# Kernel tuning notes

Hardware: AMD Instinct MI355X
Metric: run time of the kernel (lower is better)

## Reference

```python
import jax, jax.numpy as jnp
import numpy as np

B, S, HID = 2, 2048, 2048
NH = 16
HD = HID // NH  # 128


def setup_inputs() -> dict:
    key = jax.random.key(0)
    ks = jax.random.split(key, 12)
    sc = 0.02
    return {
        "hidden_state": jax.random.normal(ks[0], (B, S, HID), jnp.float32),
        "attention_mask": jax.random.uniform(ks[1], (B, 1, S, S), jnp.float32),
        "Wq": jax.random.normal(ks[2], (HID, HID), jnp.float32) * sc,
        "bq": jnp.zeros((HID,), jnp.float32),
        "Wk": jax.random.normal(ks[3], (HD, HID), jnp.float32) * sc,
        "bk": jnp.zeros((HD,), jnp.float32),
        "Wv": jax.random.normal(ks[4], (HD, HID), jnp.float32) * sc,
        "bv": jnp.zeros((HD,), jnp.float32),
        "Wo": jax.random.normal(ks[5], (HID, HID), jnp.float32) * sc,
        "bo": jnp.zeros((HID,), jnp.float32),
    }


def reference(hidden_state, attention_mask, Wq, bq, Wk, bk, Wv, bv, Wo, bo):
    b = hidden_state.shape[0]
    # projections (nn.Linear: x @ W.T + b)
    q = hidden_state @ Wq.T + bq                      # [B,S,HID]
    k = hidden_state @ Wk.T + bk                      # [B,S,HD] (single shared head)
    v = hidden_state @ Wv.T + bv                      # [B,S,HD]
    # split heads: q -> [B,NH,S,HD]
    q = q.reshape(b, -1, NH, HD).transpose(0, 2, 1, 3)
    scale = jnp.sqrt(jnp.asarray(HD, q.dtype))
    scores = jnp.einsum('bhsd,btd->bhst', q, k) / scale  # [B,NH,S,S]
    # faithful to source: mask scaled by -1e-09 (as written)
    scores = scores + attention_mask * (-1e-09)
    probs = jax.nn.softmax(scores, axis=-1)
    out = jnp.einsum('bhst,btd->bhsd', probs, v)          # [B,NH,S,HD]
    # faithful to source: transpose(-1,-2) then flat view to [B,S,HID]
    out = out.transpose(0, 1, 3, 2).reshape(b, -1, HD * NH)
    return out @ Wo.T + bo
```

## Files before the change

kernel.cpp:

```cpp
#include <hip/hip_runtime.h>
#include <hip/hip_bf16.h>

#define BATCH 2
#define SEQ 2048
#define HIDDIM 2048
#define NHEADS 16
#define HDIM 128
#define QKVN 2304

typedef __attribute__((ext_vector_type(8))) short bf16x8;
typedef __attribute__((ext_vector_type(4))) short short4v;
typedef __attribute__((ext_vector_type(4))) float f32x4;
typedef __attribute__((ext_vector_type(16))) float f32x16;
typedef __attribute__((ext_vector_type(4))) unsigned u32x4;

__device__ __forceinline__ short f2bf(float f) {
  unsigned u = __builtin_bit_cast(unsigned, f);
  unsigned r = (u + 0x7fffu + ((u >> 16) & 1u)) >> 16;
  return (short)r;
}

__device__ __forceinline__ unsigned cvtpk_bf16(float a, float b) {
  unsigned r;
  asm("v_cvt_pk_bf16_f32 %0, %1, %2" : "=v"(r) : "v"(a), "v"(b));
  return r;
}

#define PLSWAP(a, b) asm("v_permlane32_swap_b32 %0, %1" : "+v"(a), "+v"(b))

__device__ __forceinline__ void gl_lds16(const void* g, void* l) {
  __builtin_amdgcn_global_load_lds(
      (const __attribute__((address_space(1))) void*)g,
      (__attribute__((address_space(3))) void*)l, 16, 0, 0);
}

__device__ __forceinline__ float max3f(float a, float b, float c) {
  return fmaxf(fmaxf(a, b), c);
}
__device__ __forceinline__ float vmax16(const f32x16& v) {
  float a = max3f(v[0], v[1], v[2]);
  float b = max3f(v[3], v[4], v[5]);
  float c = max3f(v[6], v[7], v[8]);
  float d = max3f(v[9], v[10], v[11]);
  float e = max3f(v[12], v[13], v[14]);
  return fmaxf(max3f(a, b, c), max3f(d, e, v[15]));
}

__global__ void prep_kernel(const float* __restrict__ h, const float* __restrict__ Wq,
                            const float* __restrict__ Wk, const float* __restrict__ Wv,
                            const float* __restrict__ Wo,
                            const float* __restrict__ bq, const float* __restrict__ bk,
                            const float* __restrict__ bv,
                            short* __restrict__ h_bf, short* __restrict__ Wqkv_bf,
                            short* __restrict__ Wo_bf, float* __restrict__ bqkv)
{
  int bid = blockIdx.x;
  const float* src;
  short* dst;
  int n;
  if (bid < 8192)        { src = h;  dst = h_bf;                n = 8388608; }
  else if (bid < 12288)  { src = Wq; dst = Wqkv_bf;             n = 4194304; bid -= 8192; }
  else if (bid < 12544)  { src = Wk; dst = Wqkv_bf + 4194304;   n = 262144;  bid -= 12288; }
  else if (bid < 12800)  { src = Wv; dst = Wqkv_bf + 4456448;   n = 262144;  bid -= 12544; }
  else if (bid < 12809) {
    int i = (bid - 12800) * 256 + threadIdx.x;
    if (i < QKVN) {
      float v;
      if (i < HIDDIM) v = bq[i];
      else if (i < HIDDIM + HDIM) v = bk[i - HIDDIM];
      else v = bv[i - HIDDIM - HDIM];
      bqkv[i] = v;
    }
    return;
  }
  else                   { src = Wo; dst = Wo_bf;               n = 4194304; bid -= 12809; }
  int i = (bid * 256 + threadIdx.x) * 4;
  if (i >= n) return;
  float4 v = *(const float4*)(src + i);
  short4v o;
  o[0] = f2bf(v.x); o[1] = f2bf(v.y); o[2] = f2bf(v.z); o[3] = f2bf(v.w);
  *(short4v*)(dst + i) = o;
}

__global__ void cvt_kernel(const float* __restrict__ in, short* __restrict__ out, int n) {
  int i = (blockIdx.x * blockDim.x + threadIdx.x) * 4;
  if (i >= n) return;
  float4 v = *(const float4*)(in + i);
  short4v o;
  o[0] = f2bf(v.x); o[1] = f2bf(v.y); o[2] = f2bf(v.z); o[3] = f2bf(v.w);
  *(short4v*)(out + i) = o;
}

template <int MODE>
__global__ __launch_bounds__(256, 2)
void gemm_bt(const short* __restrict__ A, const short* __restrict__ W,
             const float* __restrict__ bias, void* __restrict__ Cv, void* __restrict__ Cv2,
             int M, int N, int K, long sA, long sC)
{
  __shared__ short As[128 * 64];
  __shared__ short Ws[128 * 64];
  const int tid = threadIdx.x;
  const int lane = tid & 63;
  const int w = tid >> 6;
  const int wr = w >> 1, wc = w & 1;
  const int tm = blockIdx.y * 128, tn = blockIdx.x * 128;
  const short* Ap = A + (size_t)blockIdx.z * sA;

  const int rA = lane & 15;
  const int r7 = rA & 7;
  const int srow = lane >> 3;
  const int scg  = (lane & 7) ^ srow;

  f32x4 acc[4][4] = {};

  for (int k0 = 0; k0 < K; k0 += 64) {
    __syncthreads();
#pragma unroll
    for (int i = 0; i < 4; ++i) {
      int ch = w * 4 + i;
      gl_lds16(Ap + (size_t)(tm + ch * 8 + srow) * K + k0 + scg * 8, As + ch * 512);
      gl_lds16(W  + (size_t)(tn + ch * 8 + srow) * K + k0 + scg * 8, Ws + ch * 512);
    }
    __syncthreads();
#pragma unroll
    for (int kk = 0; kk < 64; kk += 32) {
      const int cg = (kk >> 3) + (lane >> 4);
      const int co = ((cg ^ r7) << 3);
      bf16x8 af[4];
#pragma unroll
      for (int mi = 0; mi < 4; ++mi)
        af[mi] = *(const bf16x8*)(As + ((wr * 64 + mi * 16 + rA) << 6) + co);
#pragma unroll
      for (int ni = 0; ni < 4; ++ni) {
        bf16x8 wf = *(const bf16x8*)(Ws + ((wc * 64 + ni * 16 + rA) << 6) + co);
#pragma unroll
        for (int mi = 0; mi < 4; ++mi)
          acc[mi][ni] = __builtin_amdgcn_mfma_f32_16x16x32_bf16(af[mi], wf, acc[mi][ni], 0, 0, 0);
      }
    }
  }

  const float QSCALE = 0.12752600954427384f;
  const int cr = (lane >> 4) * 4;
  const int cc = lane & 15;
#pragma unroll
  for (int ni = 0; ni < 4; ++ni) {
    int col = tn + wc * 64 + ni * 16 + cc;
    float bv = bias[col];
#pragma unroll
    for (int mi = 0; mi < 4; ++mi) {
#pragma unroll
      for (int r = 0; r < 4; ++r) {
        int row = tm + wr * 64 + mi * 16 + cr + r;
        float v = acc[mi][ni][r] + bv;
        if constexpr (MODE == 0) {
          ((float*)Cv)[(size_t)blockIdx.z * sC + (size_t)row * N + col] = v;
        } else {
          if (col < HIDDIM)
            ((short*)Cv)[(size_t)row * QKVN + col] = f2bf(v * QSCALE);
          else if (col < HIDDIM + HDIM)
            ((short*)Cv)[(size_t)row * QKVN + col] = f2bf(v);
          else
            ((short*)Cv2)[(size_t)(col - HIDDIM - HDIM) * (BATCH * SEQ) + row] = f2bf(v);
        }
      }
    }
  }
}

__global__ __launch_bounds__(256, 2)
void attn_kernel(const short* __restrict__ QKV, const short* __restrict__ Vt,
                 short* __restrict__ OT)
{
  __shared__ short smem[32768];
  short* Ks = smem;
  short* Vs = smem + 16384;
  const int tid = threadIdx.x;
  const int l31 = tid & 31;
  const int hi2 = (tid >> 5) & 1;
  const int w = tid >> 6;
  const int b = blockIdx.z, h = blockIdx.y, qt = blockIdx.x;
  const int rx = l31 & 15;
  const short* Kp = QKV + HIDDIM;

  const short* kptr[8];
  const short* vptr[8];
  {
    const int rin = (tid & 63) >> 4;
    const int gp = tid & 15;
#pragma unroll
    for (int i = 0; i < 8; ++i) {
      int ch = w * 8 + i;
      int row = ch * 4 + rin;
      int gl = gp ^ (row & 15);
      kptr[i] = Kp + (size_t)(b * SEQ + row) * QKVN + gl * 8;
      vptr[i] = Vt + (size_t)row * (BATCH * SEQ) + b * SEQ + gl * 8;
    }
  }

  bf16x8 qf[8];
  {
    const short* Qp = QKV + (size_t)(b * SEQ + qt * 128 + w * 32 + l31) * QKVN + h * HDIM;
#pragma unroll
    for (int kk = 0; kk < 8; ++kk)
      qf[kk] = *(const bf16x8*)(Qp + kk * 16 + hi2 * 8);
  }

  f32x16 o[4] = {};
  float m = -1e30f, l = 0.f;

  for (int c = 0; c < 16; ++c) {
    __syncthreads();
#pragma unroll
    for (int i = 0; i < 8; ++i) {
      int ch = w * 8 + i;
      gl_lds16(kptr[i], Ks + ch * 512);
      gl_lds16(vptr[i], Vs + ch * 512);
      kptr[i] += 128 * QKVN;
      vptr[i] += 128;
    }
    __syncthreads();

    f32x16 s[4] = {};
    __builtin_amdgcn_s_setprio(1);
#pragma unroll
    for (int n = 0; n < 4; ++n) {
      const int row = n * 32 + l31;
#pragma unroll
      for (int kk = 0; kk < 8; ++kk) {
        bf16x8 kf = *(const bf16x8*)(Ks + row * 128 + (((kk * 2 + hi2) ^ rx) << 3));
        s[n] = __builtin_amdgcn_mfma_f32_32x32x16_bf16(kf, qf[kk], s[n], 0, 0, 0);
      }
    }
    __builtin_amdgcn_s_setprio(0);

    float mx = fmaxf(fmaxf(vmax16(s[0]), vmax16(s[1])),
                     fmaxf(vmax16(s[2]), vmax16(s[3])));
    mx = fmaxf(mx, __shfl_xor(mx, 32));
    if (!__all(mx <= m + 8.f)) {
      float mn = fmaxf(m, mx);
      float cf = __builtin_amdgcn_exp2f(m - mn);
      m = mn; l *= cf;
#pragma unroll
      for (int nd = 0; nd < 4; ++nd)
#pragma unroll
        for (int r = 0; r < 16; ++r) o[nd][r] *= cf;
    }

    float rs = 0.f;
#pragma unroll
    for (int n = 0; n < 4; ++n) {
      float p[16];
#pragma unroll
      for (int r = 0; r < 16; ++r)
        p[r] = __builtin_amdgcn_exp2f(s[n][r] - m);
      rs += (((p[0] + p[1]) + (p[2] + p[3])) + ((p[4] + p[5]) + (p[6] + p[7])))
          + (((p[8] + p[9]) + (p[10] + p[11])) + ((p[12] + p[13]) + (p[14] + p[15])));
      unsigned w0 = cvtpk_bf16(p[0], p[1]),  w1 = cvtpk_bf16(p[2], p[3]);
      unsigned w2 = cvtpk_bf16(p[4], p[5]),  w3 = cvtpk_bf16(p[6], p[7]);
      unsigned w4 = cvtpk_bf16(p[8], p[9]),  w5 = cvtpk_bf16(p[10], p[11]);
      unsigned w6 = cvtpk_bf16(p[12], p[13]), w7 = cvtpk_bf16(p[14], p[15]);
      PLSWAP(w0, w2); PLSWAP(w1, w3);
      PLSWAP(w4, w6); PLSWAP(w5, w7);
      bf16x8 pa0 = __builtin_bit_cast(bf16x8, (u32x4){w0, w1, w2, w3});
      bf16x8 pa1 = __builtin_bit_cast(bf16x8, (u32x4){w4, w5, w6, w7});
      __builtin_amdgcn_s_setprio(1);
#pragma unroll
      for (int nd = 0; nd < 4; ++nd) {
        const int row = nd * 32 + l31;
        bf16x8 vf0 = *(const bf16x8*)(Vs + row * 128 + ((((n * 2) * 2 + hi2) ^ rx) << 3));
        o[nd] = __builtin_amdgcn_mfma_f32_32x32x16_bf16(vf0, pa0, o[nd], 0, 0, 0);
        bf16x8 vf1 = *(const bf16x8*)(Vs + row * 128 + ((((n * 2 + 1) * 2 + hi2) ^ rx) << 3));
        o[nd] = __builtin_amdgcn_mfma_f32_32x32x16_bf16(vf1, pa1, o[nd], 0, 0, 0);
      }
      __builtin_amdgcn_s_setprio(0);
    }
    rs += __shfl_xor(rs, 32);
    l += rs;
  }

  const float inv = 1.f / l;
  short* dst = OT + (size_t)b * (SEQ * HIDDIM) + (size_t)(h * HDIM) * SEQ
             + qt * 128 + w * 32 + l31;
#pragma unroll
  for (int nd = 0; nd < 4; ++nd) {
#pragma unroll
    for (int r = 0; r < 16; ++r) {
      int d = nd * 32 + (r & 3) + 8 * (r >> 2) + 4 * hi2;
      dst[(size_t)d * SEQ] = f2bf(o[nd][r] * inv);
    }
  }
}

extern "C" void kernel_launch(void* const* d_in, const int* in_sizes, int n_in,
                              void* d_out, int out_size, void* d_ws, size_t ws_size,
                              hipStream_t stream)
{
  const float* hidden = (const float*)d_in[0];
  const float* Wq = (const float*)d_in[2];
  const float* bq = (const float*)d_in[3];
  const float* Wk = (const float*)d_in[4];
  const float* bk = (const float*)d_in[5];
  const float* Wv = (const float*)d_in[6];
  const float* bv = (const float*)d_in[7];
  const float* Wo = (const float*)d_in[8];
  const float* bo = (const float*)d_in[9];
  float* out = (float*)d_out;

  short* ws      = (short*)d_ws;
  short* QKV     = ws;
  short* Vt_bf   = ws + 9437184;
  short* h_bf    = Vt_bf + 524288;
  short* OT      = h_bf;
  short* Wqkv_bf = h_bf + 8388608;
  float* bqkv    = (float*)(Wqkv_bf + 4718592);
  short* Wo_sep  = (short*)(bqkv + QKVN);

  const bool sep = ws_size >= (size_t)54535168;
  short* Wo_bf = sep ? Wo_sep : QKV;

  prep_kernel<<<sep ? 16905 : 12809, 256, 0, stream>>>(
      hidden, Wq, Wk, Wv, Wo, bq, bk, bv, h_bf, Wqkv_bf, Wo_bf, bqkv);

  gemm_bt<3><<<dim3(18, 32, 1), 256, 0, stream>>>(h_bf, Wqkv_bf, bqkv, QKV, Vt_bf,
                                                  4096, QKVN, 2048, 0, 0);
  attn_kernel<<<dim3(16, 16, 2), 256, 0, stream>>>(QKV, Vt_bf, OT);
  if (!sep) cvt_kernel<<<4096, 256, 0, stream>>>(Wo, Wo_bf, 4194304);
  gemm_bt<0><<<dim3(16, 16, 2), 256, 0, stream>>>(OT, Wo_bf, bo, out, nullptr,
                                                  2048, 2048, 2048, 4194304, 4194304);
}
```

Baseline: 188.3 us.

## Pipeline attention with triple-buffered 64-key tiles and 256-row query blocks

The attention kernel now uses 512-thread blocks that each cover 256 query rows, so every loaded K/V tile feeds twice as many rows. The key loop steps in 64-key tiles through a three-slot LDS ring, and it is software-pipelined: the next tile's load and the next QK^T run while softmax and PV run on the current tile. This aims to hide global-to-LDS latency and halve K/V reloads per query. The cost is more LDS (96KB per block), more registers for the second score set, and half as many blocks in the grid.

```diff
diff --git a/kernel.cpp b/kernel.cpp
--- a/kernel.cpp
+++ b/kernel.cpp
@@ -168,14 +168,13 @@
   }
 }
 
-__global__ __launch_bounds__(256, 2)
+__global__ __launch_bounds__(512, 2)
 void attn_kernel(const short* __restrict__ QKV, const short* __restrict__ Vt,
                  short* __restrict__ OT)
 {
-  __shared__ short smem[32768];
-  short* Ks = smem;
-  short* Vs = smem + 16384;
+  __shared__ short smem[49152];
   const int tid = threadIdx.x;
+  const int lane = tid & 63;
   const int l31 = tid & 31;
   const int hi2 = (tid >> 5) & 1;
   const int w = tid >> 6;
@@ -183,105 +182,132 @@
   const int rx = l31 & 15;
   const short* Kp = QKV + HIDDIM;
 
-  const short* kptr[8];
-  const short* vptr[8];
+  const short *kp0, *kp1, *vp0, *vp1;
+  int dK0, dK1, dV0, dV1;
   {
-    const int rin = (tid & 63) >> 4;
-    const int gp = tid & 15;
-#pragma unroll
-    for (int i = 0; i < 8; ++i) {
-      int ch = w * 8 + i;
-      int row = ch * 4 + rin;
-      int gl = gp ^ (row & 15);
-      kptr[i] = Kp + (size_t)(b * SEQ + row) * QKVN + gl * 8;
-      vptr[i] = Vt + (size_t)row * (BATCH * SEQ) + b * SEQ + gl * 8;
-    }
+    int s0 = w * 128 + lane, s1 = s0 + 64;
+    int r0 = s0 >> 4, g0 = (s0 & 15) ^ (r0 & 15);
+    int r1 = s1 >> 4, g1 = (s1 & 15) ^ (r1 & 15);
+    kp0 = Kp + (size_t)(b * SEQ + r0) * QKVN + g0 * 8;
+    kp1 = Kp + (size_t)(b * SEQ + r1) * QKVN + g1 * 8;
+    int d0 = (g0 >> 3) * 64 + r0, e0 = g0 & 7;
+    int d1 = (g1 >> 3) * 64 + r1, e1 = g1 & 7;
+    vp0 = Vt + (size_t)d0 * (BATCH * SEQ) + b * SEQ + e0 * 8;
+    vp1 = Vt + (size_t)d1 * (BATCH * SEQ) + b * SEQ + e1 * 8;
+    dK0 = w * 1024;        dK1 = dK0 + 512;
+    dV0 = 8192 + dK0;      dV1 = 8192 + dK1;
   }
 
   bf16x8 qf[8];
   {
-    const short* Qp = QKV + (size_t)(b * SEQ + qt * 128 + w * 32 + l31) * QKVN + h * HDIM;
+    const short* Qp = QKV + (size_t)(b * SEQ + qt * 256 + w * 32 + l31) * QKVN + h * HDIM;
 #pragma unroll
     for (int kk = 0; kk < 8; ++kk)
       qf[kk] = *(const bf16x8*)(Qp + kk * 16 + hi2 * 8);
   }
 
   f32x16 o[4] = {};
+  f32x16 sA[2], sB[2];
   float m = -1e30f, l = 0.f;
 
-  for (int c = 0; c < 16; ++c) {
+#define STAGE(BUF)                                                         \
+  { short* nb = smem + (BUF) * 16384;                                      \
+    gl_lds16(kp0, nb + dK0); gl_lds16(kp1, nb + dK1);                      \
+    gl_lds16(vp0, nb + dV0); gl_lds16(vp1, nb + dV1);                      \
+    kp0 += 64 * QKVN; kp1 += 64 * QKVN; vp0 += 64; vp1 += 64; }
+
+#define QKT(SN, BUF)                                                       \
+  { const short* KsN = smem + (BUF) * 16384;                               \
+    SN[0] = (f32x16){}; SN[1] = (f32x16){};                                \
+    __builtin_amdgcn_s_setprio(1);                                         \
+    _Pragma("unroll")                                                      \
+    for (int n = 0; n < 2; ++n) {                                          \
+      const int row = n * 32 + l31;                                        \
+      _Pragma("unroll")                                                    \
+      for (int kk = 0; kk < 8; ++kk) {                                     \
+        bf16x8 kf = *(const bf16x8*)(KsN + row * 128 +                     \
+                                     (((kk * 2 + hi2) ^ rx) << 3));        \
+        SN[n] = __builtin_amdgcn_mfma_f32_32x32x16_bf16(kf, qf[kk], SN[n], 0, 0, 0); \
+      }                                                                    \
+    }                                                                      \
+    __builtin_amdgcn_s_setprio(0); }
+
+#define SOFT(SC)                                                           \
+  { float mx = fmaxf(vmax16(SC[0]), vmax16(SC[1]));                        \
+    mx = fmaxf(mx, __shfl_xor(mx, 32));                                    \
+    if (!__all(mx <= m + 8.f)) {                                           \
+      float mn = fmaxf(m, mx);                                             \
+      float cf = __builtin_amdgcn_exp2f(m - mn);                           \
+      m = mn; l *= cf;                                                     \
+      _Pragma("unroll")                                                    \
+      for (int nd = 0; nd < 4; ++nd)                                       \
+        _Pragma("unroll")                                                  \
+        for (int r = 0; r < 16; ++r) o[nd][r] *= cf;                       \
+    } }
+
+#define PACKPV(SC, BUF)                                                    \
+  { const short* Vs = smem + (BUF) * 16384 + 8192;                         \
+    float rs = 0.f;                                                        \
+    _Pragma("unroll")                                                      \
+    for (int n = 0; n < 2; ++n) {                                          \
+      float p[16];                                                         \
+      _Pragma("unroll")                                                    \
+      for (int r = 0; r < 16; ++r)                                         \
+        p[r] = __builtin_amdgcn_exp2f(SC[n][r] - m);                       \
+      rs += (((p[0] + p[1]) + (p[2] + p[3])) + ((p[4] + p[5]) + (p[6] + p[7])))  \
+          + (((p[8] + p[9]) + (p[10] + p[11])) + ((p[12] + p[13]) + (p[14] + p[15]))); \
+      unsigned w0 = cvtpk_bf16(p[0], p[1]),  w1 = cvtpk_bf16(p[2], p[3]);  \
+      unsigned w2 = cvtpk_bf16(p[4], p[5]),  w3 = cvtpk_bf16(p[6], p[7]);  \
+      unsigned w4 = cvtpk_bf16(p[8], p[9]),  w5 = cvtpk_bf16(p[10], p[11]); \
+      unsigned w6 = cvtpk_bf16(p[12], p[13]), w7 = cvtpk_bf16(p[14], p[15]); \
+      PLSWAP(w0, w2); PLSWAP(w1, w3);                                      \
+      PLSWAP(w4, w6); PLSWAP(w5, w7);                                      \
+      bf16x8 pa0 = __builtin_bit_cast(bf16x8, (u32x4){w0, w1, w2, w3});    \
+      bf16x8 pa1 = __builtin_bit_cast(bf16x8, (u32x4){w4, w5, w6, w7});    \
+      __builtin_amdgcn_s_setprio(1);                                       \
+      _Pragma("unroll")                                                    \
+      for (int nd = 0; nd < 4; ++nd) {                                     \
+        const int r2 = (nd & 1) * 32 + l31;                                \
+        const int ph = (nd >> 1) * 8;                                      \
+        bf16x8 vf0 = *(const bf16x8*)(Vs + r2 * 128 +                      \
+                     (((ph + (n * 2) * 2 + hi2) ^ rx) << 3));              \
+        o[nd] = __builtin_amdgcn_mfma_f32_32x32x16_bf16(vf0, pa0, o[nd], 0, 0, 0); \
+        bf16x8 vf1 = *(const bf16x8*)(Vs + r2 * 128 +                      \
+                     (((ph + (n * 2 + 1) * 2 + hi2) ^ rx) << 3));          \
+        o[nd] = __builtin_amdgcn_mfma_f32_32x32x16_bf16(vf1, pa1, o[nd], 0, 0, 0); \
+      }                                                                    \
+      __builtin_amdgcn_s_setprio(0);                                       \
+    }                                                                      \
+    rs += __shfl_xor(rs, 32); l += rs; }
+
+  STAGE(0);
+  __syncthreads();
+  STAGE(1);
+  QKT(sA, 0);
+  __syncthreads();
+
+  for (int t = 0; t < 15; ++t) {
+    const int c = 2 * t;
+    STAGE((c + 2) % 3);
+    QKT(sB, (c + 1) % 3);
+    SOFT(sA);
+    PACKPV(sA, c % 3);
     __syncthreads();
-#pragma unroll
-    for (int i = 0; i < 8; ++i) {
-      int ch = w * 8 + i;
-      gl_lds16(kptr[i], Ks + ch * 512);
-      gl_lds16(vptr[i], Vs + ch * 512);
-      kptr[i] += 128 * QKVN;
-      vptr[i] += 128;
-    }
+    STAGE((c + 3) % 3);
+    QKT(sA, (c + 2) % 3);
+    SOFT(sB);
+    PACKPV(sB, (c + 1) % 3);
     __syncthreads();
-
-    f32x16 s[4] = {};
-    __builtin_amdgcn_s_setprio(1);
-#pragma unroll
-    for (int n = 0; n < 4; ++n) {
-      const int row = n * 32 + l31;
-#pragma unroll
-      for (int kk = 0; kk < 8; ++kk) {
-        bf16x8 kf = *(const bf16x8*)(Ks + row * 128 + (((kk * 2 + hi2) ^ rx) << 3));
-        s[n] = __builtin_amdgcn_mfma_f32_32x32x16_bf16(kf, qf[kk], s[n], 0, 0, 0);
-      }
-    }
-    __builtin_amdgcn_s_setprio(0);
-
-    float mx = fmaxf(fmaxf(vmax16(s[0]), vmax16(s[1])),
-                     fmaxf(vmax16(s[2]), vmax16(s[3])));
-    mx = fmaxf(mx, __shfl_xor(mx, 32));
-    if (!__all(mx <= m + 8.f)) {
-      float mn = fmaxf(m, mx);
-      float cf = __builtin_amdgcn_exp2f(m - mn);
-      m = mn; l *= cf;
-#pragma unroll
-      for (int nd = 0; nd < 4; ++nd)
-#pragma unroll
-        for (int r = 0; r < 16; ++r) o[nd][r] *= cf;
-    }
-
-    float rs = 0.f;
-#pragma unroll
-    for (int n = 0; n < 4; ++n) {
-      float p[16];
-#pragma unroll
-      for (int r = 0; r < 16; ++r)
-        p[r] = __builtin_amdgcn_exp2f(s[n][r] - m);
-      rs += (((p[0] + p[1]) + (p[2] + p[3])) + ((p[4] + p[5]) + (p[6] + p[7])))
-          + (((p[8] + p[9]) + (p[10] + p[11])) + ((p[12] + p[13]) + (p[14] + p[15])));
-      unsigned w0 = cvtpk_bf16(p[0], p[1]),  w1 = cvtpk_bf16(p[2], p[3]);
-      unsigned w2 = cvtpk_bf16(p[4], p[5]),  w3 = cvtpk_bf16(p[6], p[7]);
-      unsigned w4 = cvtpk_bf16(p[8], p[9]),  w5 = cvtpk_bf16(p[10], p[11]);
-      unsigned w6 = cvtpk_bf16(p[12], p[13]), w7 = cvtpk_bf16(p[14], p[15]);
-      PLSWAP(w0, w2); PLSWAP(w1, w3);
-      PLSWAP(w4, w6); PLSWAP(w5, w7);
-      bf16x8 pa0 = __builtin_bit_cast(bf16x8, (u32x4){w0, w1, w2, w3});
-      bf16x8 pa1 = __builtin_bit_cast(bf16x8, (u32x4){w4, w5, w6, w7});
-      __builtin_amdgcn_s_setprio(1);
-#pragma unroll
-      for (int nd = 0; nd < 4; ++nd) {
-        const int row = nd * 32 + l31;
-        bf16x8 vf0 = *(const bf16x8*)(Vs + row * 128 + ((((n * 2) * 2 + hi2) ^ rx) << 3));
-        o[nd] = __builtin_amdgcn_mfma_f32_32x32x16_bf16(vf0, pa0, o[nd], 0, 0, 0);
-        bf16x8 vf1 = *(const bf16x8*)(Vs + row * 128 + ((((n * 2 + 1) * 2 + hi2) ^ rx) << 3));
-        o[nd] = __builtin_amdgcn_mfma_f32_32x32x16_bf16(vf1, pa1, o[nd], 0, 0, 0);
-      }
-      __builtin_amdgcn_s_setprio(0);
-    }
-    rs += __shfl_xor(rs, 32);
-    l += rs;
-  }
+  }
+  QKT(sB, 31 % 3);
+  SOFT(sA);
+  PACKPV(sA, 30 % 3);
+  SOFT(sB);
+  PACKPV(sB, 31 % 3);
 
   const float inv = 1.f / l;
   short* dst = OT + (size_t)b * (SEQ * HIDDIM) + (size_t)(h * HDIM) * SEQ
-             + qt * 128 + w * 32 + l31;
+             + qt * 256 + w * 32 + l31;
 #pragma unroll
   for (int nd = 0; nd < 4; ++nd) {
 #pragma unroll
@@ -290,6 +316,10 @@
       dst[(size_t)d * SEQ] = f2bf(o[nd][r] * inv);
     }
   }
+#undef STAGE
+#undef QKT
+#undef SOFT
+#undef PACKPV
 }
 
 extern "C" void kernel_launch(void* const* d_in, const int* in_sizes, int n_in,
@@ -324,7 +354,7 @@
 
   gemm_bt<3><<<dim3(18, 32, 1), 256, 0, stream>>>(h_bf, Wqkv_bf, bqkv, QKV, Vt_bf,
                                                   4096, QKVN, 2048, 0, 0);
-  attn_kernel<<<dim3(16, 16, 2), 256, 0, stream>>>(QKV, Vt_bf, OT);
+  attn_kernel<<<dim3(8, 16, 2), 512, 0, stream>>>(QKV, Vt_bf, OT);
   if (!sep) cvt_kernel<<<4096, 256, 0, stream>>>(Wo, Wo_bf, 4194304);
   gemm_bt<0><<<dim3(16, 16, 2), 256, 0, stream>>>(OT, Wo_bf, bo, out, nullptr,
                                                   2048, 2048, 2048, 4194304, 4194304);
```

Result: no change. 186.5 us (-0.9%).
